# Optimization experiments

Hardware: AMD Instinct MI355X
Metric: run time of the kernel (lower is better)

Reference implementation:

```python
import jax, jax.numpy as jnp
import numpy as np

H, D = 24, 128
HID = H * D  # 3072
IP_DIM = 2048
B, S_IMG, S_TXT, L_IP = 1, 1024, 512, 16
EPS = 1e-6
IP_SCALE = 1.0


def _rms(x, w):
    v = jnp.mean(jnp.square(x), axis=-1, keepdims=True)
    return x * jax.lax.rsqrt(v + EPS) * w


def _heads(x):
    b, s, _ = x.shape
    return x.reshape(b, s, H, D).transpose(0, 2, 1, 3)  # [b,H,s,D]


def _unheads(x):
    b, h, s, d = x.shape
    return x.transpose(0, 2, 1, 3).reshape(b, s, h * d)


def _rope(x, cos, sin):
    # diffusers flux apply_rotary_emb (use_real, unbind_dim=-1): interleaved pairs
    xr = x.reshape(x.shape[:-1] + (D // 2, 2))
    xrot = jnp.stack([-xr[..., 1], xr[..., 0]], axis=-1).reshape(x.shape)
    return x * cos + xrot * sin


def _sdpa(q, k, v):
    scale = 1.0 / jnp.sqrt(jnp.asarray(D, q.dtype))
    s = jnp.einsum('bhqd,bhkd->bhqk', q, k) * scale
    return jnp.einsum('bhqk,bhkd->bhqd', jax.nn.softmax(s, axis=-1), v)


def setup_inputs() -> dict:
    ks = iter(jax.random.split(jax.random.key(0), 24))
    std = 0.02
    lin = lambda k, di, do: std * jax.random.normal(k, (di, do), jnp.float32)
    z = lambda: jnp.zeros((HID,), jnp.float32)
    ones = lambda: jnp.ones((D,), jnp.float32)
    return {
        'hidden_states': jax.random.normal(next(ks), (B, S_IMG, HID), jnp.float32),
        'encoder_hidden_states': jax.random.normal(next(ks), (B, S_TXT, HID), jnp.float32),
        'ip_hidden_states': jax.random.normal(next(ks), (B, L_IP, IP_DIM), jnp.float32),
        'rope_cos': jax.random.uniform(next(ks), (S_TXT + S_IMG, D), jnp.float32),
        'rope_sin': jax.random.uniform(next(ks), (S_TXT + S_IMG, D), jnp.float32),
        'Wq': lin(next(ks), HID, HID), 'bq': z(),
        'Wk': lin(next(ks), HID, HID), 'bk': z(),
        'Wv': lin(next(ks), HID, HID), 'bv': z(),
        'norm_q_w': ones(), 'norm_k_w': ones(),
        'Waq': lin(next(ks), HID, HID), 'baq': z(),
        'Wak': lin(next(ks), HID, HID), 'bak': z(),
        'Wav': lin(next(ks), HID, HID), 'bav': z(),
        'norm_added_q_w': ones(), 'norm_added_k_w': ones(),
        'Wo': lin(next(ks), HID, HID), 'bo': z(),
        'Wadd_out': lin(next(ks), HID, HID), 'badd_out': z(),
        'Wk_ip': lin(next(ks), IP_DIM, HID), 'bk_ip': z(),
        'Wv_ip': lin(next(ks), IP_DIM, HID), 'bv_ip': z(),
        'norm_ip_q_w': ones(), 'norm_ip_k_w': ones(),
    }


def reference(hidden_states, encoder_hidden_states, ip_hidden_states, rope_cos, rope_sin,
              Wq, bq, Wk, bk, Wv, bv, norm_q_w, norm_k_w,
              Waq, baq, Wak, bak, Wav, bav, norm_added_q_w, norm_added_k_w,
              Wo, bo, Wadd_out, badd_out,
              Wk_ip, bk_ip, Wv_ip, bv_ip, norm_ip_q_w, norm_ip_k_w):
    s_txt = encoder_hidden_states.shape[1]
    # image-token projections
    q = hidden_states @ Wq + bq
    k = hidden_states @ Wk + bk
    v = hidden_states @ Wv + bv

    # IP-adapter cross-attention branch (uses q pre-RMSNorm / pre-RoPE)
    ip_q = _rms(_heads(q), norm_ip_q_w)                               # [B,H,S_img,D]
    ip_k = _rms(_heads(ip_hidden_states @ Wk_ip + bk_ip), norm_ip_k_w)  # [B,H,L_ip,D]
    ip_v = _heads(ip_hidden_states @ Wv_ip + bv_ip)
    ip_out = _unheads(_sdpa(ip_q, ip_k, ip_v))                        # [B,S_img,HID]

    qh = _rms(_heads(q), norm_q_w)
    kh = _rms(_heads(k), norm_k_w)
    vh = _heads(v)

    # text-token (encoder) projections
    eq = _rms(_heads(encoder_hidden_states @ Waq + baq), norm_added_q_w)
    ek = _rms(_heads(encoder_hidden_states @ Wak + bak), norm_added_k_w)
    ev = _heads(encoder_hidden_states @ Wav + bav)

    qf = _rope(jnp.concatenate([eq, qh], axis=2), rope_cos, rope_sin)
    kf = _rope(jnp.concatenate([ek, kh], axis=2), rope_cos, rope_sin)
    vf = jnp.concatenate([ev, vh], axis=2)

    out = _unheads(_sdpa(qf, kf, vf))                                 # [B,S_txt+S_img,HID]
    enc_out, img_out = out[:, :s_txt], out[:, s_txt:]
    img_out = img_out + ip_out * IP_SCALE
    img_out = img_out @ Wo + bo
    enc_out = enc_out @ Wadd_out + badd_out
    return (img_out, enc_out)
```

## Files before the change

### kernel.cpp

```cpp
#include <hip/hip_runtime.h>

typedef __bf16 bf16x8 __attribute__((ext_vector_type(8)));
typedef float f32x4 __attribute__((ext_vector_type(4)));
typedef unsigned short u16;
typedef unsigned int u32;

#define QSCALE 0.08838834764831845f

static __device__ __forceinline__ float bf2f(u16 u) {
  union { float f; u32 i; } x; x.i = ((u32)u) << 16; return x.f;
}
static __device__ __forceinline__ u16 f2bf(float f) {
  union { float f; u32 i; } x; x.f = f;
  u32 r = x.i + 0x7fffu + ((x.i >> 16) & 1u);
  return (u16)(r >> 16);
}
static __device__ __forceinline__ void gload16(const void* gp, void* lp) {
  __builtin_amdgcn_global_load_lds(
      (const __attribute__((address_space(1))) u32*)gp,
      (__attribute__((address_space(3))) u32*)lp, 16, 0, 0);
}

__global__ __launch_bounds__(256) void k_conv_acts(
    const float* __restrict__ hs, const float* __restrict__ ehs, const float* __restrict__ iph,
    u16* __restrict__ hsb, u16* __restrict__ ehsb, u16* __restrict__ ipb)
{
  int i = blockIdx.x * 256 + threadIdx.x;
  const float* s; u16* d; int j;
  if (i < 786432)        { s = hs;  d = hsb;  j = i; }
  else if (i < 1179648)  { s = ehs; d = ehsb; j = i - 786432; }
  else                   { s = iph; d = ipb;  j = i - 1179648; }
  float4 v = ((const float4*)s)[j];
  uint2 o;
  o.x = (u32)f2bf(v.x) | ((u32)f2bf(v.y) << 16);
  o.y = (u32)f2bf(v.z) | ((u32)f2bf(v.w) << 16);
  ((uint2*)d)[j] = o;
}

struct WT { const float* src; u16* dst; int K; };
struct WTPack { WT w[10]; };

__global__ __launch_bounds__(256) void k_transp_w(WTPack p)
{
  WT d = p.w[blockIdx.z];
  int K = d.K;
  int k0 = blockIdx.y * 64;
  if (k0 >= K) return;
  int n0 = blockIdx.x * 64;
  __shared__ u16 T[64 * 72];
  int tid = threadIdx.x;
  #pragma unroll
  for (int i = 0; i < 4; i++) {
    int idx = tid + i * 256;
    int r = idx >> 4, ch = idx & 15;
    float4 v = *(const float4*)(d.src + (size_t)(k0 + r) * 3072 + n0 + ch * 4);
    T[(ch*4+0)*72 + r] = f2bf(v.x);
    T[(ch*4+1)*72 + r] = f2bf(v.y);
    T[(ch*4+2)*72 + r] = f2bf(v.z);
    T[(ch*4+3)*72 + r] = f2bf(v.w);
  }
  __syncthreads();
  #pragma unroll
  for (int i = 0; i < 2; i++) {
    int idx = tid + i * 256;
    int r = idx >> 3, ch = idx & 7;
    uint4 v = *(const uint4*)(T + r * 72 + ch * 8);
    *(uint4*)(d.dst + (size_t)(n0 + r) * K + k0 + ch * 8) = v;
  }
}

struct GJob { const u16* A; const u16* W; const float* bias; void* C; int M; int K; int blk0; int out_f32; };
struct GPack { GJob j[8]; int njobs; };

template<int MT>
__global__ __launch_bounds__(256) void k_gemm(GPack p)
{
  __shared__ u16 As[MT * 64];
  __shared__ u16 Bs[128 * 64];
  int bid = blockIdx.x;
  int ji = 0;
  while (ji + 1 < p.njobs && bid >= p.j[ji+1].blk0) ji++;
  GJob J = p.j[ji];
  int local = bid - J.blk0;
  int m0 = (local / 24) * MT;
  int n0 = (local % 24) * 128;

  int tid = threadIdx.x, w = tid >> 6, lane = tid & 63, l15 = lane & 15, quad = lane >> 4;
  constexpr int MF = MT / 32;
  int wm = (w >> 1) * (MT / 2), wn = (w & 1) * 64;
  f32x4 acc[MF][4] = {};

  constexpr int GA = MT * 8 / 256;
  const u16* Ag[GA]; const u16* Bg[4];
  #pragma unroll
  for (int i = 0; i < GA; i++) {
    int s = i * 256 + tid;
    int row = s >> 3, kc = (s & 7) ^ (row & 7);
    Ag[i] = J.A + (size_t)(m0 + row) * J.K + kc * 8;
  }
  #pragma unroll
  for (int i = 0; i < 4; i++) {
    int s = i * 256 + tid;
    int row = s >> 3, kc = (s & 7) ^ (row & 7);
    Bg[i] = J.W + (size_t)(n0 + row) * J.K + kc * 8;
  }

  for (int k0 = 0; k0 < J.K; k0 += 64) {
    #pragma unroll
    for (int i = 0; i < GA; i++)
      gload16(Ag[i] + k0, As + (size_t)(i * 256 + w * 64) * 8);
    #pragma unroll
    for (int i = 0; i < 4; i++)
      gload16(Bg[i] + k0, Bs + (size_t)(i * 256 + w * 64) * 8);
    __syncthreads();
    int x7 = l15 & 7;
    #pragma unroll
    for (int ks = 0; ks < 2; ks++) {
      bf16x8 af[MF], bfr[4];
      #pragma unroll
      for (int t = 0; t < MF; t++)
        af[t] = *(const bf16x8*)(As + (wm + t * 16 + l15) * 64 + (((ks * 4 + quad) ^ x7) * 8));
      #pragma unroll
      for (int t = 0; t < 4; t++)
        bfr[t] = *(const bf16x8*)(Bs + (wn + t * 16 + l15) * 64 + (((ks * 4 + quad) ^ x7) * 8));
      #pragma unroll
      for (int mt = 0; mt < MF; mt++)
        #pragma unroll
        for (int nt = 0; nt < 4; nt++)
          acc[mt][nt] = __builtin_amdgcn_mfma_f32_16x16x32_bf16(af[mt], bfr[nt], acc[mt][nt], 0, 0, 0);
    }
    __syncthreads();
  }

  #pragma unroll
  for (int mt = 0; mt < MF; mt++) {
    int row = m0 + wm + mt * 16 + quad * 4;
    #pragma unroll
    for (int nt = 0; nt < 4; nt++) {
      int col = n0 + wn + nt * 16 + l15;
      float bv = J.bias[col];
      #pragma unroll
      for (int r = 0; r < 4; r++) {
        if (row + r < J.M) {
          float v = acc[mt][nt][r] + bv;
          if (J.out_f32) ((float*)J.C)[(size_t)(row + r) * 3072 + col] = v;
          else           ((u16*)J.C)[(size_t)(row + r) * 3072 + col] = f2bf(v);
        }
      }
    }
  }
}

__global__ __launch_bounds__(256) void k_pack_qk(
    const u16* __restrict__ q, const u16* __restrict__ k,
    const u16* __restrict__ eq, const u16* __restrict__ ek,
    const u16* __restrict__ ipk,
    const float* __restrict__ cosr, const float* __restrict__ sinr,
    const float* __restrict__ nq, const float* __restrict__ nk,
    const float* __restrict__ naq, const float* __restrict__ nak,
    const float* __restrict__ nipq, const float* __restrict__ nipk,
    u16* __restrict__ Qf, u16* __restrict__ Kf, u16* __restrict__ Qip, u16* __restrict__ Kip)
{
  int u = blockIdx.x * 4 + (threadIdx.x >> 6);
  int lane = threadIdx.x & 63;
  int d0 = lane * 2;
  if (u < 36864) {
    int t = u / 24, h = u % 24;
    bool txt = t < 512;
    const u16* qrow = txt ? eq + (size_t)t * 3072 : q + (size_t)(t - 512) * 3072;
    const u16* krow = txt ? ek + (size_t)t * 3072 : k + (size_t)(t - 512) * 3072;
    u32 qv = ((const u32*)(qrow + h * 128))[lane];
    u32 kv = ((const u32*)(krow + h * 128))[lane];
    float q0 = bf2f((u16)qv), q1 = bf2f((u16)(qv >> 16));
    float k0 = bf2f((u16)kv), k1 = bf2f((u16)(kv >> 16));
    float sq = q0 * q0 + q1 * q1, sk = k0 * k0 + k1 * k1;
    #pragma unroll
    for (int off = 32; off > 0; off >>= 1) {
      sq += __shfl_xor(sq, off, 64);
      sk += __shfl_xor(sk, off, 64);
    }
    float rq = rsqrtf(sq * (1.0f / 128.0f) + 1e-6f);
    float rk = rsqrtf(sk * (1.0f / 128.0f) + 1e-6f);
    const float* wq = txt ? naq : nq;
    const float* wk = txt ? nak : nk;
    float2 c = ((const float2*)(cosr + (size_t)t * 128))[lane];
    float2 s = ((const float2*)(sinr + (size_t)t * 128))[lane];
    float xq0 = q0 * rq * wq[d0] * QSCALE, xq1 = q1 * rq * wq[d0 + 1] * QSCALE;
    float xk0 = k0 * rk * wk[d0],          xk1 = k1 * rk * wk[d0 + 1];
    u32 oq = (u32)f2bf(xq0 * c.x - xq1 * s.x) | ((u32)f2bf(xq1 * c.y + xq0 * s.y) << 16);
    u32 ok = (u32)f2bf(xk0 * c.x - xk1 * s.x) | ((u32)f2bf(xk1 * c.y + xk0 * s.y) << 16);
    ((u32*)(Qf + ((size_t)h * 1536 + t) * 128))[lane] = oq;
    ((u32*)(Kf + ((size_t)h * 1536 + t) * 128))[lane] = ok;
    if (!txt) {
      float y0 = q0 * rq * nipq[d0] * QSCALE, y1 = q1 * rq * nipq[d0 + 1] * QSCALE;
      u32 oy = (u32)f2bf(y0) | ((u32)f2bf(y1) << 16);
      ((u32*)(Qip + ((size_t)h * 1024 + (t - 512)) * 128))[lane] = oy;
    }
  } else {
    int u2 = u - 36864;
    if (u2 < 384) {
      int h = u2 >> 4, t = u2 & 15;
      u32 v = ((const u32*)(ipk + (size_t)t * 3072 + h * 128))[lane];
      float x0 = bf2f((u16)v), x1 = bf2f((u16)(v >> 16));
      float ss = x0 * x0 + x1 * x1;
      #pragma unroll
      for (int off = 32; off > 0; off >>= 1) ss += __shfl_xor(ss, off, 64);
      float rr = rsqrtf(ss * (1.0f / 128.0f) + 1e-6f);
      u32 o = (u32)f2bf(x0 * rr * nipk[d0]) | ((u32)f2bf(x1 * rr * nipk[d0 + 1]) << 16);
      ((u32*)(Kip + ((size_t)h * 64 + t) * 128))[lane] = o;
    }
  }
}

__global__ __launch_bounds__(256) void k_pack_v(
    const u16* __restrict__ v, const u16* __restrict__ ev, const u16* __restrict__ ipv,
    u16* __restrict__ Vt, u16* __restrict__ Vipt)
{
  __shared__ u16 T[64 * 72];
  int h = blockIdx.x, y = blockIdx.y, tid = threadIdx.x;
  if (y < 48) {
    int tb = (y % 24) * 64, db = (y / 24) * 64;
    #pragma unroll
    for (int i = 0; i < 2; i++) {
      int idx = tid + i * 256;
      int r = idx >> 3, ch = idx & 7;
      int t = tb + r;
      const u16* src = (t < 512) ? ev + (size_t)t * 3072 : v + (size_t)(t - 512) * 3072;
      uint4 val = *(const uint4*)(src + h * 128 + db + ch * 8);
      u16 tmp[8];
      *(uint4*)tmp = val;
      #pragma unroll
      for (int j = 0; j < 8; j++) T[(ch * 8 + j) * 72 + r] = tmp[j];
    }
    __syncthreads();
    #pragma unroll
    for (int i = 0; i < 2; i++) {
      int idx = tid + i * 256;
      int r = idx >> 3, ch = idx & 7;
      uint4 val = *(const uint4*)(T + r * 72 + ch * 8);
      *(uint4*)(Vt + ((size_t)h * 128 + db + r) * 1536 + tb + ch * 8) = val;
    }
  } else {
    if (tid < 128) {
      #pragma unroll
      for (int t = 0; t < 64; t++) {
        u16 val = 0;
        if (t < 16) val = ipv[(size_t)t * 3072 + h * 128 + tid];
        Vipt[((size_t)h * 128 + tid) * 64 + t] = val;
      }
    }
  }
}

__global__ __launch_bounds__(256) void k_attn(
    const u16* __restrict__ Q, const u16* __restrict__ K, const u16* __restrict__ V,
    const float* __restrict__ addend, void* __restrict__ out,
    int Sq, int Skv, int Skv_valid, int mode)
{
  __shared__ u16 Ks[64 * 128];
  __shared__ u16 Vs[128 * 64];
  __shared__ u16 Ps[4 * 16 * 68];
  int tid = threadIdx.x, h = blockIdx.y;
  int w = tid >> 6, lane = tid & 63, l15 = lane & 15, quad = lane >> 4;
  int mb = blockIdx.x * 64 + w * 16;

  bf16x8 aq[4];
  {
    const u16* qp = Q + ((size_t)h * Sq + mb + l15) * 128 + quad * 8;
    #pragma unroll
    for (int c = 0; c < 4; c++) aq[c] = *(const bf16x8*)(qp + c * 32);
  }

  const u16* Kg[4]; const u16* Vg[4];
  #pragma unroll
  for (int i = 0; i < 4; i++) {
    int s = tid + i * 256;
    int key = s >> 4, kc = (s & 15) ^ (key & 15);
    Kg[i] = K + ((size_t)h * Skv + key) * 128 + kc * 8;
    int d = s >> 3, vc = (s & 7) ^ (d & 7);
    Vg[i] = V + ((size_t)h * 128 + d) * Skv + vc * 8;
  }

  f32x4 o[8] = {};
  float m_col = -3.0e38f, l_col = 0.0f;
  u16* myPs = Ps + w * (16 * 68);

  for (int kb = 0; kb < Skv; kb += 64) {
    #pragma unroll
    for (int i = 0; i < 4; i++) {
      gload16(Kg[i] + (size_t)kb * 128, Ks + (i * 256 + w * 64) * 8);
      gload16(Vg[i] + kb,               Vs + (i * 256 + w * 64) * 8);
    }
    __syncthreads();

    f32x4 sc[4];
    #pragma unroll
    for (int mt = 0; mt < 4; mt++) {
      f32x4 a = {0.f, 0.f, 0.f, 0.f};
      int key = mt * 16 + l15;
      #pragma unroll
      for (int c = 0; c < 4; c++) {
        bf16x8 kf = *(const bf16x8*)(Ks + key * 128 + (((c * 4 + quad) ^ l15) * 8));
        a = __builtin_amdgcn_mfma_f32_16x16x32_bf16(kf, aq[c], a, 0, 0, 0);
      }
      sc[mt] = a;
    }
    if (Skv_valid != Skv) {
      #pragma unroll
      for (int mt = 0; mt < 4; mt++)
        #pragma unroll
        for (int r = 0; r < 4; r++)
          if (kb + mt * 16 + quad * 4 + r >= Skv_valid) sc[mt][r] = -1e30f;
    }

    float mx = sc[0][0];
    #pragma unroll
    for (int mt = 0; mt < 4; mt++)
      #pragma unroll
      for (int r = 0; r < 4; r++) mx = fmaxf(mx, sc[mt][r]);
    mx = fmaxf(mx, __shfl_xor(mx, 16, 64));
    mx = fmaxf(mx, __shfl_xor(mx, 32, 64));
    float mn = fmaxf(m_col, mx);
    float alpha = __expf(m_col - mn);
    m_col = mn;

    float sum = 0.f;
    #pragma unroll
    for (int mt = 0; mt < 4; mt++) {
      u16 pk[4];
      #pragma unroll
      for (int r = 0; r < 4; r++) {
        float pp = __expf(sc[mt][r] - mn);
        sum += pp;
        pk[r] = f2bf(pp);
      }
      uint2 pv;
      pv.x = (u32)pk[0] | ((u32)pk[1] << 16);
      pv.y = (u32)pk[2] | ((u32)pk[3] << 16);
      *(uint2*)(myPs + l15 * 68 + mt * 16 + quad * 4) = pv;
    }
    sum += __shfl_xor(sum, 16, 64);
    sum += __shfl_xor(sum, 32, 64);
    l_col = l_col * alpha + sum;

    float ar[4];
    #pragma unroll
    for (int r = 0; r < 4; r++) ar[r] = __shfl(alpha, quad * 4 + r, 64);
    #pragma unroll
    for (int nt = 0; nt < 8; nt++) {
      o[nt][0] *= ar[0]; o[nt][1] *= ar[1]; o[nt][2] *= ar[2]; o[nt][3] *= ar[3];
    }

    __asm__ volatile("s_waitcnt lgkmcnt(0)" ::: "memory");
    #pragma unroll
    for (int kc = 0; kc < 2; kc++) {
      bf16x8 pa = *(const bf16x8*)(myPs + l15 * 68 + kc * 32 + quad * 8);
      #pragma unroll
      for (int nt = 0; nt < 8; nt++) {
        int d = nt * 16 + l15;
        bf16x8 vf = *(const bf16x8*)(Vs + d * 64 + (((kc * 4 + quad) ^ (d & 7)) * 8));
        o[nt] = __builtin_amdgcn_mfma_f32_16x16x32_bf16(pa, vf, o[nt], 0, 0, 0);
      }
    }
    __syncthreads();
  }

  float linv = 1.0f / l_col;
  float lr[4];
  #pragma unroll
  for (int r = 0; r < 4; r++) lr[r] = __shfl(linv, quad * 4 + r, 64);
  #pragma unroll
  for (int r = 0; r < 4; r++) {
    int t = mb + quad * 4 + r;
    size_t base = (size_t)t * 3072 + h * 128 + l15;
    if (mode == 0) {
      float* O = (float*)out;
      #pragma unroll
      for (int nt = 0; nt < 8; nt++) O[base + nt * 16] = o[nt][r] * lr[r];
    } else {
      u16* O = (u16*)out;
      #pragma unroll
      for (int nt = 0; nt < 8; nt++) {
        float vv = o[nt][r] * lr[r];
        if (t >= 512) vv += addend[(size_t)(t - 512) * 3072 + h * 128 + nt * 16 + l15];
        O[base + nt * 16] = f2bf(vv);
      }
    }
  }
}

extern "C" void kernel_launch(void* const* d_in, const int* in_sizes, int n_in,
                              void* d_out, int out_size, void* d_ws, size_t ws_size,
                              hipStream_t stream) {
  const float* hs   = (const float*)d_in[0];
  const float* ehs  = (const float*)d_in[1];
  const float* iph  = (const float*)d_in[2];
  const float* cosr = (const float*)d_in[3];
  const float* sinr = (const float*)d_in[4];
  const float* Wq   = (const float*)d_in[5];  const float* bq   = (const float*)d_in[6];
  const float* Wk   = (const float*)d_in[7];  const float* bk   = (const float*)d_in[8];
  const float* Wv   = (const float*)d_in[9];  const float* bv   = (const float*)d_in[10];
  const float* nq   = (const float*)d_in[11]; const float* nk   = (const float*)d_in[12];
  const float* Waq  = (const float*)d_in[13]; const float* baq  = (const float*)d_in[14];
  const float* Wak  = (const float*)d_in[15]; const float* bak  = (const float*)d_in[16];
  const float* Wav  = (const float*)d_in[17]; const float* bav  = (const float*)d_in[18];
  const float* naq  = (const float*)d_in[19]; const float* nak  = (const float*)d_in[20];
  const float* Wo   = (const float*)d_in[21]; const float* bo   = (const float*)d_in[22];
  const float* Wad  = (const float*)d_in[23]; const float* bad  = (const float*)d_in[24];
  const float* Wkip = (const float*)d_in[25]; const float* bkip = (const float*)d_in[26];
  const float* Wvip = (const float*)d_in[27]; const float* bvip = (const float*)d_in[28];
  const float* nipq = (const float*)d_in[29]; const float* nipk = (const float*)d_in[30];
  (void)in_sizes; (void)n_in; (void)out_size; (void)ws_size;

  char* ws = (char*)d_ws;
  size_t off = 0;
  auto alloc = [&](size_t bytes) { size_t o = off; off += (bytes + 255) & ~(size_t)255; return o; };

  u16* hsb  = (u16*)(ws + alloc((size_t)1024 * 3072 * 2));
  u16* ehsb = (u16*)(ws + alloc((size_t)512 * 3072 * 2));
  u16* ipb  = (u16*)(ws + alloc((size_t)16 * 2048 * 2));
  u16* WT_[10];
  for (int i = 0; i < 10; i++) WT_[i] = (u16*)(ws + alloc((size_t)3072 * (i < 8 ? 3072 : 2048) * 2));
  u16* qb   = (u16*)(ws + alloc((size_t)1024 * 3072 * 2));
  u16* kb_  = (u16*)(ws + alloc((size_t)1024 * 3072 * 2));
  u16* vb   = (u16*)(ws + alloc((size_t)1024 * 3072 * 2));
  u16* eqb  = (u16*)(ws + alloc((size_t)512 * 3072 * 2));
  u16* ekb  = (u16*)(ws + alloc((size_t)512 * 3072 * 2));
  u16* evb  = (u16*)(ws + alloc((size_t)512 * 3072 * 2));
  u16* ipkb = (u16*)(ws + alloc((size_t)16 * 3072 * 2));
  u16* ipvb = (u16*)(ws + alloc((size_t)16 * 3072 * 2));
  u16* Qf   = (u16*)(ws + alloc((size_t)24 * 1536 * 128 * 2));
  u16* Kff  = (u16*)(ws + alloc((size_t)24 * 1536 * 128 * 2));
  u16* Vt   = (u16*)(ws + alloc((size_t)24 * 128 * 1536 * 2));
  u16* Qip  = (u16*)(ws + alloc((size_t)24 * 1024 * 128 * 2));
  u16* Kip  = (u16*)(ws + alloc((size_t)24 * 64 * 128 * 2));
  u16* Vipt = (u16*)(ws + alloc((size_t)24 * 128 * 64 * 2));
  float* ip_out = (float*)(ws + alloc((size_t)1024 * 3072 * 4));
  u16* attnb = (u16*)(ws + alloc((size_t)1536 * 3072 * 2));

  k_conv_acts<<<4640, 256, 0, stream>>>(hs, ehs, iph, hsb, ehsb, ipb);

  WTPack p;
  const float* wsrc[10] = {Wq, Wk, Wv, Waq, Wak, Wav, Wo, Wad, Wkip, Wvip};
  for (int i = 0; i < 10; i++) { p.w[i].src = wsrc[i]; p.w[i].dst = WT_[i]; p.w[i].K = (i < 8 ? 3072 : 2048); }
  k_transp_w<<<dim3(48, 48, 10), 256, 0, stream>>>(p);

  {
    GPack pp;
    const u16* As_[8]  = {hsb, hsb, hsb, ehsb, ehsb, ehsb, ipb, ipb};
    const u16* Ws_[8]  = {WT_[0], WT_[1], WT_[2], WT_[3], WT_[4], WT_[5], WT_[8], WT_[9]};
    const float* bs_[8] = {bq, bk, bv, baq, bak, bav, bkip, bvip};
    u16* Cs_[8]        = {qb, kb_, vb, eqb, ekb, evb, ipkb, ipvb};
    int Ms_[8] = {1024, 1024, 1024, 512, 512, 512, 16, 16};
    int Ks_[8] = {3072, 3072, 3072, 3072, 3072, 3072, 2048, 2048};
    int blk = 0;
    for (int i = 0; i < 8; i++) {
      pp.j[i].A = As_[i]; pp.j[i].W = Ws_[i]; pp.j[i].bias = bs_[i]; pp.j[i].C = Cs_[i];
      pp.j[i].M = Ms_[i]; pp.j[i].K = Ks_[i]; pp.j[i].blk0 = blk; pp.j[i].out_f32 = 0;
      blk += ((Ms_[i] + 127) / 128) * 24;
    }
    pp.njobs = 8;
    k_gemm<128><<<dim3(blk), 256, 0, stream>>>(pp);
  }

  k_pack_qk<<<9312, 256, 0, stream>>>(qb, kb_, eqb, ekb, ipkb, cosr, sinr, nq, nk, naq, nak, nipq, nipk, Qf, Kff, Qip, Kip);
  k_pack_v<<<dim3(24, 49), 256, 0, stream>>>(vb, evb, ipvb, Vt, Vipt);

  k_attn<<<dim3(16, 24), 256, 0, stream>>>(Qip, Kip, Vipt, (const float*)nullptr, ip_out, 1024, 64, 16, 0);
  k_attn<<<dim3(24, 24), 256, 0, stream>>>(Qf, Kff, Vt, ip_out, attnb, 1536, 1536, 1536, 1);

  {
    GPack pp;
    float* out = (float*)d_out;
    pp.j[0].A = attnb + (size_t)512 * 3072; pp.j[0].W = WT_[6]; pp.j[0].bias = bo;
    pp.j[0].C = out; pp.j[0].M = 1024; pp.j[0].K = 3072; pp.j[0].blk0 = 0; pp.j[0].out_f32 = 1;
    pp.j[1].A = attnb; pp.j[1].W = WT_[7]; pp.j[1].bias = bad;
    pp.j[1].C = out + (size_t)1024 * 3072; pp.j[1].M = 512; pp.j[1].K = 3072;
    pp.j[1].blk0 = (1024 / 64) * 24; pp.j[1].out_f32 = 1;
    pp.njobs = 2;
    k_gemm<64><<<dim3((1024 / 64) * 24 + (512 / 64) * 24), 256, 0, stream>>>(pp);
  }
}
```

Baseline: 725.8 us.

## Replace QKV projection GEMM with 256x256-tile 8-wave pipelined kernel

Adds a new GEMM kernel for the batched input projections. It uses 256x256 output tiles with 512 threads and 128 KB of dynamic LDS. Loads go straight from global memory to LDS, double-buffered with swizzled columns, over a four-phase loop that overlaps the next K-slab loads with MFMA work. Block indices are remapped in an XCD-aware order. The larger tiles are meant to raise arithmetic intensity and cut the number of blocks; the cost is low occupancy, only 240 blocks, and a mapping hardcoded to that block count. The small 16-row IP jobs now use 256-row tiles and read past their rows.

```diff
diff --git a/kernel.cpp b/kernel.cpp
--- a/kernel.cpp
+++ b/kernel.cpp
@@ -67,6 +67,104 @@
     uint4 v = *(const uint4*)(T + r * 72 + ch * 8);
     *(uint4*)(d.dst + (size_t)(n0 + r) * K + k0 + ch * 8) = v;
   }
+}
+
+struct G8Job { const u16* A; const u16* W; const float* bias; void* C; int M; int K; int blk0; int out_f32; };
+struct G8Pack { G8Job j[8]; int njobs; };
+
+__global__ __launch_bounds__(512, 2) void k_gemm8(G8Pack p)
+{
+  extern __shared__ __align__(16) u16 smem[];
+  u16* As = smem;
+  u16* Bs = smem + 32768;
+
+  int bid = blockIdx.x;
+  bid = (bid & 7) * 30 + (bid >> 3);
+  int ji = 0;
+  while (ji + 1 < p.njobs && bid >= p.j[ji + 1].blk0) ji++;
+  G8Job J = p.j[ji];
+  int local = bid - J.blk0;
+  int m0 = (local / 12) * 256;
+  int n0 = (local % 12) * 256;
+  int K = J.K, NT = K >> 6;
+
+  int tid = threadIdx.x, w = tid >> 6, lane = tid & 63, l15 = lane & 15, quad = lane >> 4;
+  int wm = (w >> 2) * 128, wn = (w & 3) * 64;
+  int dw = w * 512;
+  int cread = (quad ^ (l15 & 3)) * 8;
+
+  int rr = tid >> 2;
+  int c4 = ((tid & 3) ^ (rr & 3)) * 8;
+  const u16* pa0 = J.A + (size_t)(m0 + rr) * K + c4;
+  const u16* pa1 = pa0 + (size_t)128 * K;
+  const u16* pb0 = J.W + (size_t)(n0 + rr) * K + c4;
+  const u16* pb1 = pb0 + (size_t)128 * K;
+
+  f32x4 acc[8][4] = {};
+  bf16x8 af[4], bfr[4];
+
+#define STAGE_A(b, kh, tt) do { int _ko = (tt) * 64 + (kh) * 32; int _d = ((b) * 2 + (kh)) * 8192 + dw; \
+    gload16(pa0 + _ko, As + _d); gload16(pa1 + _ko, As + _d + 4096); } while (0)
+#define STAGE_B(b, kh, tt) do { int _ko = (tt) * 64 + (kh) * 32; int _d = ((b) * 2 + (kh)) * 8192 + dw; \
+    gload16(pb0 + _ko, Bs + _d); gload16(pb1 + _ko, Bs + _d + 4096); } while (0)
+
+  STAGE_A(0, 0, 0); STAGE_B(0, 0, 0); STAGE_A(0, 1, 0); STAGE_B(0, 1, 0);
+  STAGE_A(1, 0, 1); STAGE_B(1, 0, 1);
+  __asm__ volatile("s_waitcnt vmcnt(4)" ::: "memory");
+  __builtin_amdgcn_s_barrier();
+
+#define PHASE(ks, mtb, READB, STAGES, WAITS) do { \
+    int _ab = (cur * 2 + (ks)) * 8192; \
+    _Pragma("unroll") for (int i = 0; i < 4; i++) \
+      af[i] = *(const bf16x8*)(As + _ab + (wm + ((mtb) + i) * 16 + l15) * 32 + cread); \
+    if (READB) { _Pragma("unroll") for (int i = 0; i < 4; i++) \
+      bfr[i] = *(const bf16x8*)(Bs + _ab + (wn + i * 16 + l15) * 32 + cread); } \
+    STAGES; WAITS; \
+    __builtin_amdgcn_s_barrier(); \
+    __asm__ volatile("s_waitcnt lgkmcnt(0)" ::: "memory"); \
+    __builtin_amdgcn_sched_barrier(0); \
+    __builtin_amdgcn_s_setprio(1); \
+    _Pragma("unroll") for (int mt = 0; mt < 4; mt++) \
+      _Pragma("unroll") for (int nt = 0; nt < 4; nt++) \
+        acc[(mtb) + mt][nt] = __builtin_amdgcn_mfma_f32_16x16x32_bf16(af[mt], bfr[nt], acc[(mtb) + mt][nt], 0, 0, 0); \
+    __builtin_amdgcn_s_setprio(0); \
+    __builtin_amdgcn_sched_barrier(0); \
+    __builtin_amdgcn_s_barrier(); \
+  } while (0)
+
+  int cur = 0;
+  for (int t = 0; t < NT; t++) {
+    int o = cur ^ 1;
+    int t1 = (t + 1 < NT) ? t + 1 : NT - 1;
+    int t2 = (t + 2 < NT) ? t + 2 : NT - 1;
+    PHASE(0, 0, 1, STAGE_A(o, 1, t1), (void)0);
+    PHASE(0, 4, 0, STAGE_B(o, 1, t1), __asm__ volatile("s_waitcnt vmcnt(8)" ::: "memory"));
+    PHASE(1, 0, 1, STAGE_A(cur, 0, t2), (void)0);
+    PHASE(1, 4, 0, STAGE_B(cur, 0, t2), __asm__ volatile("s_waitcnt vmcnt(8)" ::: "memory"));
+    cur = o;
+  }
+  __asm__ volatile("s_waitcnt vmcnt(0)" ::: "memory");
+
+  #pragma unroll
+  for (int mt = 0; mt < 8; mt++) {
+    int row = m0 + wm + mt * 16 + quad * 4;
+    #pragma unroll
+    for (int nt = 0; nt < 4; nt++) {
+      int col = n0 + wn + nt * 16 + l15;
+      float bv = J.bias[col];
+      #pragma unroll
+      for (int r = 0; r < 4; r++) {
+        if (row + r < J.M) {
+          float v = acc[mt][nt][r] + bv;
+          if (J.out_f32) ((float*)J.C)[(size_t)(row + r) * 3072 + col] = v;
+          else           ((u16*)J.C)[(size_t)(row + r) * 3072 + col] = f2bf(v);
+        }
+      }
+    }
+  }
+#undef PHASE
+#undef STAGE_A
+#undef STAGE_B
 }
 
 struct GJob { const u16* A; const u16* W; const float* bias; void* C; int M; int K; int blk0; int out_f32; };
@@ -438,6 +536,12 @@
   float* ip_out = (float*)(ws + alloc((size_t)1024 * 3072 * 4));
   u16* attnb = (u16*)(ws + alloc((size_t)1536 * 3072 * 2));
 
+  static bool attr_done = false;
+  if (!attr_done) {
+    hipFuncSetAttribute((const void*)k_gemm8, hipFuncAttributeMaxDynamicSharedMemorySize, 131072);
+    attr_done = true;
+  }
+
   k_conv_acts<<<4640, 256, 0, stream>>>(hs, ehs, iph, hsb, ehsb, ipb);
 
   WTPack p;
@@ -446,7 +550,7 @@
   k_transp_w<<<dim3(48, 48, 10), 256, 0, stream>>>(p);
 
   {
-    GPack pp;
+    G8Pack pp;
     const u16* As_[8]  = {hsb, hsb, hsb, ehsb, ehsb, ehsb, ipb, ipb};
     const u16* Ws_[8]  = {WT_[0], WT_[1], WT_[2], WT_[3], WT_[4], WT_[5], WT_[8], WT_[9]};
     const float* bs_[8] = {bq, bk, bv, baq, bak, bav, bkip, bvip};
@@ -457,10 +561,10 @@
     for (int i = 0; i < 8; i++) {
       pp.j[i].A = As_[i]; pp.j[i].W = Ws_[i]; pp.j[i].bias = bs_[i]; pp.j[i].C = Cs_[i];
       pp.j[i].M = Ms_[i]; pp.j[i].K = Ks_[i]; pp.j[i].blk0 = blk; pp.j[i].out_f32 = 0;
-      blk += ((Ms_[i] + 127) / 128) * 24;
+      blk += ((Ms_[i] + 255) / 256) * 12;
     }
     pp.njobs = 8;
-    k_gemm<128><<<dim3(blk), 256, 0, stream>>>(pp);
+    k_gemm8<<<dim3(blk), 512, 131072, stream>>>(pp);
   }
 
   k_pack_qk<<<9312, 256, 0, stream>>>(qb, kb_, eqb, ekb, ipkb, cosr, sinr, nq, nk, naq, nak, nipq, nipk, Qf, Kff, Qip, Kip);
```

New measurement: 683.5 us. 1.06x faster.
